# Optimization experiments

Hardware: AMD Instinct MI355X
Metric: run time of the kernel (lower is better)

The kernel has to match this reference:

```python
import jax, jax.numpy as jnp
import numpy as np

MODEL_DIM = 1024
NUM_HEADS = 16
HEAD_DIM = MODEL_DIM // NUM_HEADS
BATCH = 16
KEY_LEN = 4096


def setup_inputs() -> dict:
    key = jax.random.key(0)
    ks = jax.random.split(key, 10)
    u = lambda k, shape: jax.random.uniform(k, shape, jnp.float32, -0.5, 0.5)
    return {
        "hidden_states": jax.random.normal(ks[0], (BATCH, 1, MODEL_DIM), jnp.float32),
        "key_value_states": jax.random.normal(ks[1], (BATCH, KEY_LEN, MODEL_DIM), jnp.float32),
        "Wq": u(ks[2], (MODEL_DIM, MODEL_DIM)), "bq": u(ks[3], (MODEL_DIM,)),
        "Wk": u(ks[4], (MODEL_DIM, MODEL_DIM)), "bk": u(ks[5], (MODEL_DIM,)),
        "Wv": u(ks[6], (MODEL_DIM, MODEL_DIM)), "bv": u(ks[7], (MODEL_DIM,)),
        "Wo": u(ks[8], (MODEL_DIM, MODEL_DIM)), "bo": u(ks[9], (MODEL_DIM,)),
    }


def reference(hidden_states, key_value_states, Wq, bq, Wk, bk, Wv, bv, Wo, bo):
    B, K = key_value_states.shape[0], key_value_states.shape[1]
    H, Dh = NUM_HEADS, HEAD_DIM
    # projections (nn.Linear: x @ W.T + b)
    q = hidden_states @ Wq.T + bq            # [B, 1, H*Dh]
    k = key_value_states @ Wk.T + bk         # [B, K, H*Dh]
    v = key_value_states @ Wv.T + bv         # [B, K, H*Dh]
    # split heads
    q = q.reshape(B, 1, H, Dh).transpose(0, 2, 1, 3)   # [B, H, 1, Dh]
    k = k.reshape(B, K, H, Dh).transpose(0, 2, 1, 3)   # [B, H, K, Dh]
    v = v.reshape(B, K, H, Dh).transpose(0, 2, 1, 3)   # [B, H, K, Dh]
    q = q / jnp.sqrt(jnp.asarray(Dh, q.dtype))
    # scores: [B, H, K] (query_len == 1, squeezed)
    scores = jnp.einsum("bhqd,bhkd->bhqk", q, k)[:, :, 0, :]
    # Hardtanh(min_val=0, max_val=1) gate instead of softmax; dropout p=0
    attn = jnp.clip(scores, 0.0, 1.0)                  # [B, H, K]
    # broadcast-multiply with value, merge heads back
    context = attn[..., None] * v                      # [B, H, K, Dh]
    context = context.transpose(0, 2, 1, 3).reshape(B, K, H * Dh)
    output = context @ Wo.T + bo                       # [B, K, model_dim]
    return output
```

## Files before the change

### kernel.cpp

```cpp
#include <hip/hip_runtime.h>
#include <hip/hip_bf16.h>
#include <stdint.h>

typedef __bf16 bf16x8 __attribute__((ext_vector_type(8)));
typedef __bf16 bf16x4 __attribute__((ext_vector_type(4)));
typedef float  f32x4  __attribute__((ext_vector_type(4)));

#define B_  16
#define KL  4096
#define D_  1024
#define NH  16
#define NROWS (B_*KL)

__device__ __forceinline__ void gload_lds16(const void* g, void* l) {
  __builtin_amdgcn_global_load_lds(
      (__attribute__((address_space(1))) void*)g,
      (__attribute__((address_space(3))) void*)l, 16, 0, 0);
}


__global__ __launch_bounds__(256) void conv_bf16_kernel(const float* __restrict__ s,
                                                        __bf16* __restrict__ d, int n4) {
  int i = blockIdx.x * 256 + threadIdx.x;
  if (i >= n4) return;
  float4 v = reinterpret_cast<const float4*>(s)[i];
  bf16x4 o;
  o[0] = (__bf16)v.x; o[1] = (__bf16)v.y; o[2] = (__bf16)v.z; o[3] = (__bf16)v.w;
  *reinterpret_cast<bf16x4*>(d + (size_t)i * 4) = o;
}

__global__ __launch_bounds__(256) void qproj_kernel(const float* __restrict__ hs,
                                                    const float* __restrict__ Wq,
                                                    const float* __restrict__ bq,
                                                    float* __restrict__ q) {
  int gid = blockIdx.x * 256 + threadIdx.x;
  int b = gid >> 10, j = gid & 1023;
  const float* x = hs + (size_t)b * D_;
  const float* w = Wq + (size_t)j * D_;
  float acc = 0.f;
  for (int i = 0; i < D_; i += 4) {
    float4 xv = *reinterpret_cast<const float4*>(x + i);
    float4 wv = *reinterpret_cast<const float4*>(w + i);
    acc += xv.x*wv.x + xv.y*wv.y + xv.z*wv.z + xv.w*wv.w;
  }
  q[gid] = (acc + bq[j]) * 0.125f;
}

__global__ __launch_bounds__(256) void wqeff_kernel(const float* __restrict__ q,
                                                    const float* __restrict__ Wk,
                                                    const float* __restrict__ bk,
                                                    __bf16* __restrict__ whi,
                                                    __bf16* __restrict__ wlo,
                                                    float* __restrict__ cb) {
  const int h = blockIdx.x, b = blockIdx.y;
  const int tid = threadIdx.x;
  __shared__ float ql[64];
  if (tid < 64) ql[tid] = q[(size_t)b * D_ + h * 64 + tid];
  __syncthreads();
  float a0 = 0, a1 = 0, a2 = 0, a3 = 0;
  for (int d = 0; d < 64; ++d) {
    float qv = ql[d];
    const float* wr = Wk + (size_t)(h * 64 + d) * D_;
    a0 += qv * wr[tid];
    a1 += qv * wr[tid + 256];
    a2 += qv * wr[tid + 512];
    a3 += qv * wr[tid + 768];
  }
  const size_t base = ((size_t)b * NH + h) * D_;
  float a[4] = {a0, a1, a2, a3};
#pragma unroll
  for (int j = 0; j < 4; ++j) {
    __bf16 hi = (__bf16)a[j];
    whi[base + j * 256 + tid] = hi;
    wlo[base + j * 256 + tid] = (__bf16)(a[j] - (float)hi);
  }
  if (tid < 64) {
    float p = ql[tid] * bk[h * 64 + tid];
    p += __shfl_down(p, 32); p += __shfl_down(p, 16); p += __shfl_down(p, 8);
    p += __shfl_down(p, 4);  p += __shfl_down(p, 2);  p += __shfl_down(p, 1);
    if (tid == 0) cb[b * NH + h] = p;
  }
}

__global__ __launch_bounds__(256) void scores_mfma_kernel(
    const float* __restrict__ kvs,
    const __bf16* __restrict__ whi,
    const __bf16* __restrict__ wlo,
    const float* __restrict__ cb,
    float* __restrict__ attn,
    __bf16* __restrict__ kvd) {
  const int b = blockIdx.y;
  const int tid = threadIdx.x;
  const int lane = tid & 63, wv = tid >> 6;
  const int r16 = lane & 15, kgrp = lane >> 4;
  const int row0 = blockIdx.x * 64 + wv * 16;
  const size_t grow = (size_t)b * KL + row0;

  const float* xrow = kvs + (grow + r16) * D_ + kgrp * 8;
  __bf16*      krow = kvd + (grow + r16) * D_ + kgrp * 8;
  const __bf16* wh = whi + ((size_t)b * NH + r16) * D_ + kgrp * 8;
  const __bf16* wl = wlo + ((size_t)b * NH + r16) * D_ + kgrp * 8;

  f32x4 acc = {};
  for (int k0 = 0; k0 < D_; k0 += 32) {
    float4 x0 = *reinterpret_cast<const float4*>(xrow + k0);
    float4 x1 = *reinterpret_cast<const float4*>(xrow + k0 + 4);
    float xs[8] = {x0.x, x0.y, x0.z, x0.w, x1.x, x1.y, x1.z, x1.w};
    bf16x8 hi, lo;
#pragma unroll
    for (int i = 0; i < 8; ++i) {
      __bf16 h = (__bf16)xs[i];
      hi[i] = h;
      lo[i] = (__bf16)(xs[i] - (float)h);
    }
    *reinterpret_cast<bf16x8*>(krow + k0) = hi;
    bf16x8 bh = *reinterpret_cast<const bf16x8*>(wh + k0);
    bf16x8 bl = *reinterpret_cast<const bf16x8*>(wl + k0);
    acc = __builtin_amdgcn_mfma_f32_16x16x32_bf16(hi, bh, acc, 0, 0, 0);
    acc = __builtin_amdgcn_mfma_f32_16x16x32_bf16(hi, bl, acc, 0, 0, 0);
    acc = __builtin_amdgcn_mfma_f32_16x16x32_bf16(lo, bh, acc, 0, 0, 0);
  }
  const float c = cb[b * NH + r16];
#pragma unroll
  for (int r = 0; r < 4; ++r) {
    const int orow = row0 + kgrp * 4 + r;
    float s = acc[r] + c;
    attn[((size_t)b * KL + orow) * NH + r16] = fminf(fmaxf(s, 0.f), 1.f);
  }
}

template <bool GATE>
__global__ __launch_bounds__(512, 2) void gemm_nt(const __bf16* __restrict__ A,
                                                  const __bf16* __restrict__ Bt,
                                                  const float* __restrict__ bias,
                                                  const float* __restrict__ gate,
                                                  void* __restrict__ Cp) {
  __shared__ __bf16 As[2][256 * 64];
  __shared__ __bf16 Bs[2][256 * 64];
  const int tid = threadIdx.x;
  const int lane = tid & 63, wid = tid >> 6;
  const int wm = wid >> 2, wn = wid & 3;
  const int r16 = lane & 15, kgrp = lane >> 4;
  const int bswz = (blockIdx.x & 7) * 128 + (blockIdx.x >> 3);
  const int m0 = (bswz >> 2) * 256;
  const int n0 = (bswz & 3) * 256;

  const int srow = lane >> 3;
  const int scol = ((lane & 7) ^ srow) * 8;

  const int sw0 = ((kgrp) ^ (r16 & 7)) * 8;
  const int sw1 = ((4 + kgrp) ^ (r16 & 7)) * 8;

  f32x4 acc[8][4] = {};

#define STAGE_HALF(dstbuf, srcp, base0, h, k0)                                  \
  {                                                                             \
    _Pragma("unroll") for (int j = 0; j < 2; ++j) {                             \
      const int c = (h) * 16 + wid * 2 + j;                                     \
      gload_lds16((srcp) + (size_t)((base0) + c * 8 + srow) * D_ + (k0) + scol, \
                  &(dstbuf)[c * 512]);                                          \
    }                                                                           \
  }

#define LOAD_BV(Bb, sw)                                                         \
  _Pragma("unroll") for (int nh = 0; nh < 2; ++nh)                              \
    _Pragma("unroll") for (int g = 0; g < 2; ++g)                               \
      bv[nh * 2 + g] = *reinterpret_cast<const bf16x8*>(                        \
          &(Bb)[(nh * 128 + wn * 32 + g * 16 + r16) * 64 + (sw)]);

#define PHASE_MFMA(Ab, mh, sw)                                                  \
  {                                                                             \
    bf16x8 av[4];                                                               \
    _Pragma("unroll") for (int f = 0; f < 4; ++f)                               \
      av[f] = *reinterpret_cast<const bf16x8*>(                                 \
          &(Ab)[((mh) * 128 + wm * 64 + f * 16 + r16) * 64 + (sw)]);            \
    __builtin_amdgcn_s_setprio(1);                                              \
    _Pragma("unroll") for (int f = 0; f < 4; ++f)                               \
      _Pragma("unroll") for (int q = 0; q < 4; ++q)                             \
        acc[(mh) * 4 + f][q] = __builtin_amdgcn_mfma_f32_16x16x32_bf16(         \
            av[f], bv[q], acc[(mh) * 4 + f][q], 0, 0, 0);                       \
    __builtin_amdgcn_s_setprio(0);                                              \
  }

  STAGE_HALF(Bs[0], Bt, n0, 0, 0);
  STAGE_HALF(Bs[0], Bt, n0, 1, 0);
  STAGE_HALF(As[0], A,  m0, 0, 0);
  STAGE_HALF(As[0], A,  m0, 1, 0);
  asm volatile("s_waitcnt vmcnt(2)" ::: "memory");
  __builtin_amdgcn_s_barrier();

  const int NT = D_ / 64;
  for (int t = 0; t < NT; ++t) {
    __bf16* Ab = (t & 1) ? As[1] : As[0];
    __bf16* Bb = (t & 1) ? Bs[1] : Bs[0];
    __bf16* An = (t & 1) ? As[0] : As[1];
    __bf16* Bn = (t & 1) ? Bs[0] : Bs[1];
    const int k1 = (t + 1) * 64;
    bf16x8 bv[4];
    if (t < NT - 1) STAGE_HALF(Bn, Bt, n0, 0, k1);
    LOAD_BV(Bb, sw0);
    PHASE_MFMA(Ab, 0, sw0);
    if (t < NT - 1) asm volatile("s_waitcnt vmcnt(2)" ::: "memory");
    else            asm volatile("s_waitcnt vmcnt(0)" ::: "memory");
    __builtin_amdgcn_s_barrier();
    if (t < NT - 1) STAGE_HALF(Bn, Bt, n0, 1, k1);
    PHASE_MFMA(Ab, 1, sw0);
    if (t < NT - 1) STAGE_HALF(An, A, m0, 0, k1);
    LOAD_BV(Bb, sw1);
    PHASE_MFMA(Ab, 0, sw1);
    if (t < NT - 1) STAGE_HALF(An, A, m0, 1, k1);
    PHASE_MFMA(Ab, 1, sw1);
    if (t < NT - 1) {
      asm volatile("s_waitcnt vmcnt(2)" ::: "memory");
      __builtin_amdgcn_s_barrier();
    }
  }

#pragma unroll
  for (int mh = 0; mh < 2; ++mh) {
#pragma unroll
    for (int f = 0; f < 4; ++f) {
      const int row0 = m0 + mh * 128 + wm * 64 + f * 16 + kgrp * 4;
#pragma unroll
      for (int nh = 0; nh < 2; ++nh) {
#pragma unroll
        for (int g = 0; g < 2; ++g) {
          const int col = n0 + nh * 128 + wn * 32 + g * 16 + r16;
          const float bc = bias[col];
          const int head = col >> 6;
          f32x4 v = acc[mh * 4 + f][nh * 2 + g];
#pragma unroll
          for (int r = 0; r < 4; ++r) {
            const int row = row0 + r;
            if constexpr (GATE) {
              float gg = gate[(size_t)row * NH + head];
              ((__bf16*)Cp)[(size_t)row * D_ + col] = (__bf16)((v[r] + bc) * gg);
            } else {
              ((float*)Cp)[(size_t)row * D_ + col] = v[r] + bc;
            }
          }
        }
      }
    }
  }
#undef STAGE_HALF
#undef LOAD_BV
#undef PHASE_MFMA
}

extern "C" void kernel_launch(void* const* d_in, const int* in_sizes, int n_in,
                              void* d_out, int out_size, void* d_ws, size_t ws_size,
                              hipStream_t stream) {
  const float* hs  = (const float*)d_in[0];
  const float* kvs = (const float*)d_in[1];
  const float* Wq  = (const float*)d_in[2];
  const float* bq  = (const float*)d_in[3];
  const float* Wk  = (const float*)d_in[4];
  const float* bk  = (const float*)d_in[5];
  const float* Wv  = (const float*)d_in[6];
  const float* bv  = (const float*)d_in[7];
  const float* Wo  = (const float*)d_in[8];
  const float* bo  = (const float*)d_in[9];
  float* out = (float*)d_out;

  char* w = (char*)d_ws;
  __bf16* ctx  = (__bf16*)w;  w += (size_t)NROWS * D_ * 2;
  float*  attn = (float*)w;   w += (size_t)NROWS * NH * 4;
  __bf16* WvB  = (__bf16*)w;  w += (size_t)D_ * D_ * 2;
  __bf16* WoB  = (__bf16*)w;  w += (size_t)D_ * D_ * 2;
  __bf16* whi  = (__bf16*)w;  w += (size_t)B_ * NH * D_ * 2;
  __bf16* wlo  = (__bf16*)w;  w += (size_t)B_ * NH * D_ * 2;
  float*  qbuf = (float*)w;   w += (size_t)B_ * D_ * 4;
  float*  cbuf = (float*)w;   w += B_ * NH * 4;

  __bf16* kvsB = (__bf16*)d_out;

  conv_bf16_kernel<<<1024, 256, 0, stream>>>(Wv, WvB, 262144);
  conv_bf16_kernel<<<1024, 256, 0, stream>>>(Wo, WoB, 262144);
  qproj_kernel<<<64, 256, 0, stream>>>(hs, Wq, bq, qbuf);
  wqeff_kernel<<<dim3(NH, B_), 256, 0, stream>>>(qbuf, Wk, bk, whi, wlo, cbuf);
  scores_mfma_kernel<<<dim3(KL / 64, B_), 256, 0, stream>>>(kvs, whi, wlo, cbuf, attn, kvsB);
  gemm_nt<true ><<<1024, 512, 0, stream>>>(kvsB, WvB, bv, attn, ctx);
  gemm_nt<false><<<1024, 512, 0, stream>>>(ctx, WoB, bo, (const float*)nullptr, (void*)out);
}
```

Before: 498.9 us.

## Restructure GEMM main loop into barrier-separated LDS-load and MFMA phases

Splits the MFMA phase macro into separate LDS fragment loads and MFMA blocks. The K-loop becomes a strict ping-pong schedule: LDS reads and global-to-LDS staging are issued, a barrier is taken, lgkmcnt is waited with a sched_barrier, then MFMAs run. The aim is to keep LDS traffic and MFMA work in distinct windows across waves, so matrix cores are not stalled by interleaved memory ops. It adds several extra barriers per iteration, which can cost more than the overlap gains if waves do not interleave well.

```diff
diff --git a/kernel.cpp b/kernel.cpp
--- a/kernel.cpp
+++ b/kernel.cpp
@@ -168,12 +168,13 @@
       bv[nh * 2 + g] = *reinterpret_cast<const bf16x8*>(                        \
           &(Bb)[(nh * 128 + wn * 32 + g * 16 + r16) * 64 + (sw)]);
 
-#define PHASE_MFMA(Ab, mh, sw)                                                  \
+#define LOAD_AV(Ab, mh, sw)                                                     \
+  _Pragma("unroll") for (int f = 0; f < 4; ++f)                                 \
+    av[f] = *reinterpret_cast<const bf16x8*>(                                   \
+        &(Ab)[((mh) * 128 + wm * 64 + f * 16 + r16) * 64 + (sw)]);
+
+#define MFMA_PHASE(mh)                                                          \
   {                                                                             \
-    bf16x8 av[4];                                                               \
-    _Pragma("unroll") for (int f = 0; f < 4; ++f)                               \
-      av[f] = *reinterpret_cast<const bf16x8*>(                                 \
-          &(Ab)[((mh) * 128 + wm * 64 + f * 16 + r16) * 64 + (sw)]);            \
     __builtin_amdgcn_s_setprio(1);                                              \
     _Pragma("unroll") for (int f = 0; f < 4; ++f)                               \
       _Pragma("unroll") for (int q = 0; q < 4; ++q)                             \
@@ -181,6 +182,10 @@
             av[f], bv[q], acc[(mh) * 4 + f][q], 0, 0, 0);                       \
     __builtin_amdgcn_s_setprio(0);                                              \
   }
+
+#define WAITLGKM()                                                              \
+  asm volatile("s_waitcnt lgkmcnt(0)" ::: "memory");                            \
+  __builtin_amdgcn_sched_barrier(0);
 
   STAGE_HALF(Bs[0], Bt, n0, 0, 0);
   STAGE_HALF(Bs[0], Bt, n0, 1, 0);
@@ -196,24 +201,38 @@
     __bf16* An = (t & 1) ? As[0] : As[1];
     __bf16* Bn = (t & 1) ? Bs[0] : Bs[1];
     const int k1 = (t + 1) * 64;
-    bf16x8 bv[4];
-    if (t < NT - 1) STAGE_HALF(Bn, Bt, n0, 0, k1);
+    const bool pf = (t < NT - 1);
+    bf16x8 bv[4], av[4];
+
     LOAD_BV(Bb, sw0);
-    PHASE_MFMA(Ab, 0, sw0);
-    if (t < NT - 1) asm volatile("s_waitcnt vmcnt(2)" ::: "memory");
-    else            asm volatile("s_waitcnt vmcnt(0)" ::: "memory");
-    __builtin_amdgcn_s_barrier();
-    if (t < NT - 1) STAGE_HALF(Bn, Bt, n0, 1, k1);
-    PHASE_MFMA(Ab, 1, sw0);
-    if (t < NT - 1) STAGE_HALF(An, A, m0, 0, k1);
+    LOAD_AV(Ab, 0, sw0);
+    if (pf) STAGE_HALF(Bn, Bt, n0, 0, k1);
+    __builtin_amdgcn_s_barrier();
+    WAITLGKM();
+    MFMA_PHASE(0);
+    if (pf) asm volatile("s_waitcnt vmcnt(2)" ::: "memory");
+    else    asm volatile("s_waitcnt vmcnt(0)" ::: "memory");
+    __builtin_amdgcn_s_barrier();
+    LOAD_AV(Ab, 1, sw0);
+    if (pf) STAGE_HALF(Bn, Bt, n0, 1, k1);
+    __builtin_amdgcn_s_barrier();
+    WAITLGKM();
+    MFMA_PHASE(1);
+    __builtin_amdgcn_s_barrier();
     LOAD_BV(Bb, sw1);
-    PHASE_MFMA(Ab, 0, sw1);
-    if (t < NT - 1) STAGE_HALF(An, A, m0, 1, k1);
-    PHASE_MFMA(Ab, 1, sw1);
-    if (t < NT - 1) {
-      asm volatile("s_waitcnt vmcnt(2)" ::: "memory");
-      __builtin_amdgcn_s_barrier();
-    }
+    LOAD_AV(Ab, 0, sw1);
+    if (pf) STAGE_HALF(An, A, m0, 0, k1);
+    __builtin_amdgcn_s_barrier();
+    WAITLGKM();
+    MFMA_PHASE(0);
+    __builtin_amdgcn_s_barrier();
+    LOAD_AV(Ab, 1, sw1);
+    if (pf) STAGE_HALF(An, A, m0, 1, k1);
+    __builtin_amdgcn_s_barrier();
+    WAITLGKM();
+    MFMA_PHASE(1);
+    if (pf) asm volatile("s_waitcnt vmcnt(2)" ::: "memory");
+    __builtin_amdgcn_s_barrier();
   }
 
 #pragma unroll
@@ -245,7 +264,9 @@
   }
 #undef STAGE_HALF
 #undef LOAD_BV
-#undef PHASE_MFMA
+#undef LOAD_AV
+#undef MFMA_PHASE
+#undef WAITLGKM
 }
 
 extern "C" void kernel_launch(void* const* d_in, const int* in_sizes, int n_in,
```

New measurement: 492.2 us, median of 3. About the same (-1.4%).
